# Kernel tuning notes

Hardware: AMD Instinct MI355X
Metric: run time of the kernel (lower is better)

## Reference

```python
import jax, jax.numpy as jnp
import numpy as np

B, N, D = 8, 1024, 512
H, DH = 8, 64
CH, CD = 6, 64  # ck/cv come in as (b, 6, n, 64); 6*64 = opn_inner_dim = 384
ID = H * DH    # inner_dim = 512
SCALE = DH ** -0.5


def _l2norm_dim1(x):
    # F.normalize(x, dim=1): normalize over the token axis of (b, n, c)
    return x / jnp.maximum(jnp.linalg.norm(x, axis=1, keepdims=True), 1e-12)


def _style_vectorizer(c, ws, bs):
    b, h, n, d = c.shape
    x = c.transpose(0, 2, 1, 3).reshape(b, n, h * d)
    x = _l2norm_dim1(x)
    for w, bi in zip(ws, bs):
        x = jax.nn.leaky_relu(x @ w.T + bi, 0.2)
    return x.reshape(b, n, H, DH).transpose(0, 2, 1, 3)


def _mlp_block(x, w, b):
    # x: (b, H, n, DH) -> rearr, normalize over n, Linear+GELU(exact), rearr back
    bb, h, n, d = x.shape
    y = x.transpose(0, 2, 1, 3).reshape(bb, n, h * d)
    y = _l2norm_dim1(y)
    y = jax.nn.gelu(y @ w.T + b, approximate=False)
    return y.reshape(bb, n, H, DH).transpose(0, 2, 1, 3)


def setup_inputs() -> dict:
    key = jax.random.key(0)
    ks = jax.random.split(key, 24)
    s = 0.02  # keep attention logits well-conditioned
    return {
        "x": jax.random.normal(ks[0], (B, N, D), jnp.float32),
        "ck": jax.random.normal(ks[1], (B, CH, N, CD), jnp.float32),
        "cv": jax.random.normal(ks[2], (B, CH, N, CD), jnp.float32),
        "w_qkv": jax.random.normal(ks[3], (3 * ID, D), jnp.float32) * s,
        "w_out": jax.random.normal(ks[4], (D, ID), jnp.float32) * s,
        "b_out": jnp.zeros((D,), jnp.float32),
        "ckw0": jax.random.normal(ks[5], (ID, CH * CD), jnp.float32) * s,
        "ckb0": jnp.zeros((ID,), jnp.float32),
        "ckw1": jax.random.normal(ks[6], (ID, ID), jnp.float32) * s,
        "ckb1": jnp.zeros((ID,), jnp.float32),
        "ckw2": jax.random.normal(ks[7], (ID, ID), jnp.float32) * s,
        "ckb2": jnp.zeros((ID,), jnp.float32),
        "cvw0": jax.random.normal(ks[8], (ID, CH * CD), jnp.float32) * s,
        "cvb0": jnp.zeros((ID,), jnp.float32),
        "cvw1": jax.random.normal(ks[9], (ID, ID), jnp.float32) * s,
        "cvb1": jnp.zeros((ID,), jnp.float32),
        "cvw2": jax.random.normal(ks[10], (ID, ID), jnp.float32) * s,
        "cvb2": jnp.zeros((ID,), jnp.float32),
        "nl_w": jax.random.normal(ks[11], (ID, ID), jnp.float32) * s,
        "nl_b": jnp.zeros((ID,), jnp.float32),
        "sub_ratio": jax.random.normal(ks[12], (1, H, 1, DH), jnp.float32) + 1.0,
    }


def reference(x, ck, cv, w_qkv, w_out, b_out,
              ckw0, ckb0, ckw1, ckb1, ckw2, ckb2,
              cvw0, cvb0, cvw1, cvb1, cvw2, cvb2,
              nl_w, nl_b, sub_ratio):
    b, n, _ = x.shape
    qkv = x @ w_qkv.T                      # (b, n, 3*ID)
    q, k, v = jnp.split(qkv, 3, axis=-1)
    to_h = lambda t: t.reshape(b, n, H, DH).transpose(0, 2, 1, 3)  # (b,H,n,DH)
    q, k, v = to_h(q), to_h(k), to_h(v)

    # standard self-attention branch
    dots = jnp.einsum("bhnd,bhmd->bhnm", q, k) * SCALE
    out = jnp.einsum("bhnm,bhmd->bhnd", jax.nn.softmax(dots, axis=-1), v)

    # context (correction) branch
    ckh = _style_vectorizer(ck, (ckw0, ckw1, ckw2), (ckb0, ckb1, ckb2))
    cvh = _style_vectorizer(cv, (cvw0, cvw1, cvw2), (cvb0, cvb1, cvb2))
    dots_c = jnp.einsum("bhnd,bhmd->bhnm", q, ckh) * SCALE
    out_c = jnp.einsum("bhnm,bhmd->bhnd", jax.nn.softmax(dots_c, axis=-1), cvh)
    out_c = _mlp_block(out_c, nl_w, nl_b)

    out = out - out_c * sub_ratio          # elementwise scale-subtract combine
    out = out.transpose(0, 2, 1, 3).reshape(b, n, ID)
    return out @ w_out.T + b_out
```

## Files before the change

### kernel.cpp

```cpp
#include <hip/hip_runtime.h>
#include <hip/hip_fp16.h>
#include <math.h>

typedef _Float16 h16_t;
typedef __attribute__((ext_vector_type(4))) _Float16 h16x4;
typedef __attribute__((ext_vector_type(8))) _Float16 h16x8;
typedef __attribute__((ext_vector_type(4))) float f32x4;

static_assert(sizeof(h16_t) == 2, "f16 size");

__device__ __forceinline__ f32x4 mfma16(h16x8 a, h16x8 b, f32x4 c) {
  return __builtin_amdgcn_mfma_f32_16x16x32_f16(a, b, c, 0, 0, 0);
}

struct CvtArgs {
  const float* src[10];
  h16_t* dst[10];
  int start4[10];
  int total4;
  int nblk_cvt;
  const float* c0;
  const float* c1;
  float* part;
};

__global__ __launch_bounds__(384) void k_cvt_p1(CvtArgs a) {
  const int bid = blockIdx.x;
  if (bid < a.nblk_cvt) {
    const int i4 = bid * 384 + threadIdx.x;
    if (i4 >= a.total4) return;
    int seg = 0;
#pragma unroll
    for (int t = 1; t < 10; ++t) seg += (i4 >= a.start4[t]) ? 1 : 0;
    const int off = (i4 - a.start4[seg]) * 4;
    const float4 v = *(const float4*)(a.src[seg] + off);
    h16x4 o;
    o[0] = (h16_t)v.x; o[1] = (h16_t)v.y; o[2] = (h16_t)v.z; o[3] = (h16_t)v.w;
    *(h16x4*)(a.dst[seg] + off) = o;
  } else {
    const int rid = bid - a.nblk_cvt;
    const int b = rid & 7, ch = (rid >> 3) & 63, z = rid >> 9;
    const int f = threadIdx.x;
    const float* c = z ? a.c1 : a.c0;
    const int h = f >> 6, d = f & 63;
    const float* p = c + ((size_t)(b * 6 + h) * 1024 + ch * 16) * 64 + d;
    float s = 0.f;
#pragma unroll
    for (int n = 0; n < 16; ++n) {
      const float v = p[(size_t)n * 64];
      s += v * v;
    }
    a.part[(size_t)z * 196608 + (size_t)(b * 64 + ch) * 384 + f] = s;
  }
}

template <int K>
__device__ __forceinline__ void gemm_run(const h16_t* __restrict__ A,
                                         const h16_t* __restrict__ W,
                                         int m0, int o0, h16_t* wl, f32x4* acc) {
  constexpr int NS = K / 128;
  const int lane = threadIdx.x & 63;
  const int l15 = lane & 15;
  const int quad = lane >> 4;
  int sr[4], sc[4], sd[4];
#pragma unroll
  for (int i = 0; i < 4; ++i) {
    const int id = threadIdx.x + i * 256;
    const int row = id >> 4, c = id & 15;
    sr[i] = row;
    sc[i] = c * 8;
    sd[i] = (row * 16 + (c ^ (row & 7))) * 8;
  }
  h16x8 wr[4];
#pragma unroll
  for (int i = 0; i < 4; ++i)
    wr[i] = *(const h16x8*)(W + (size_t)(o0 + sr[i]) * K + sc[i]);
#pragma unroll
  for (int i = 0; i < 4; ++i) *(h16x8*)(wl + sd[i]) = wr[i];
  __syncthreads();
#pragma unroll
  for (int sg = 0; sg < NS; ++sg) {
    if (sg + 1 < NS) {
#pragma unroll
      for (int i = 0; i < 4; ++i)
        wr[i] = *(const h16x8*)(W + (size_t)(o0 + sr[i]) * K + (sg + 1) * 128 + sc[i]);
    }
    const h16_t* ap = A + (size_t)(m0 + l15) * K + sg * 128 + quad * 8;
    const h16_t* wp = wl + (sg & 1) * 8192;
#pragma unroll
    for (int ks = 0; ks < 4; ++ks) {
      h16x8 af = *(const h16x8*)(ap + ks * 32);
#pragma unroll
      for (int j = 0; j < 4; ++j) {
        h16x8 wf = *(const h16x8*)(
            wp + (size_t)((j * 16 + l15) * 16 + ((ks * 4 + quad) ^ (l15 & 7))) * 8);
        acc[j] = mfma16(af, wf, acc[j]);
      }
    }
    if (sg + 1 < NS) {
      h16_t* wn = wl + ((sg + 1) & 1) * 8192;
#pragma unroll
      for (int i = 0; i < 4; ++i) *(h16x8*)(wn + sd[i]) = wr[i];
    }
    __syncthreads();
  }
}

#define EPILOGUE_SETUP()                            \
  const int wv = threadIdx.x >> 6;                  \
  const int lane = threadIdx.x & 63;                \
  const int l15 = lane & 15;                        \
  const int quad = lane >> 4;                       \
  const int m0 = blockIdx.x * 64 + wv * 16;         \
  const int o0 = blockIdx.y * 64;                   \
  f32x4 acc[4];                                     \
  for (int j = 0; j < 4; ++j) acc[j] = f32x4{0.f, 0.f, 0.f, 0.f};

struct Leaky2Args {
  const h16_t* A0; const h16_t* W0; const float* b0; h16_t* Y0;
  const h16_t* A1; const h16_t* W1; const float* b1; h16_t* Y1;
};

template <int K, int L0, int L1>
__global__ __launch_bounds__(256) void k_gemm_leaky2(Leaky2Args g) {
  __shared__ h16_t wl[2 * 8192];
  const int zz = blockIdx.z;
  const h16_t* A = zz ? g.A1 : g.A0;
  const h16_t* W = zz ? g.W1 : g.W0;
  const float* bias = zz ? g.b1 : g.b0;
  h16_t* Y = zz ? g.Y1 : g.Y0;
  EPILOGUE_SETUP();
  gemm_run<K>(A, W, m0, o0, wl, acc);
  const int LAYOUT = zz ? L1 : L0;
#pragma unroll
  for (int j = 0; j < 4; ++j)
#pragma unroll
    for (int r = 0; r < 4; ++r) {
      const int o = o0 + j * 16 + l15;
      const int m = m0 + quad * 4 + r;
      float v = acc[j][r] + bias[o];
      v = v > 0.f ? v : 0.2f * v;
      if (LAYOUT == 0) {
        Y[(size_t)m * 512 + o] = (h16_t)v;
      } else {
        const int b = m >> 10, n = m & 1023;
        const int h = o >> 6, d = o & 63;
        if (LAYOUT == 1)
          Y[((size_t)(b * 8 + h) * 1024 + n) * 64 + d] = (h16_t)v;
        else
          Y[((size_t)(b * 8 + h) * 64 + d) * 1024 + n] = (h16_t)v;
      }
    }
}

__global__ __launch_bounds__(256) void k_g0_qkv(
    Leaky2Args g, const h16_t* __restrict__ X, const h16_t* __restrict__ Wq,
    h16_t* __restrict__ qb, h16_t* __restrict__ kb, h16_t* __restrict__ vT) {
  __shared__ h16_t wl[2 * 8192];
  const int bid = blockIdx.x;
  const int wv = threadIdx.x >> 6;
  const int lane = threadIdx.x & 63;
  const int l15 = lane & 15;
  const int quad = lane >> 4;
  f32x4 acc[4];
#pragma unroll
  for (int j = 0; j < 4; ++j) acc[j] = f32x4{0.f, 0.f, 0.f, 0.f};

  if (bid < 2048) {
    const int zz = bid >> 10;
    const int m0 = (bid & 127) * 64 + wv * 16;
    const int o0 = ((bid >> 7) & 7) * 64;
    const h16_t* A = zz ? g.A1 : g.A0;
    const h16_t* W = zz ? g.W1 : g.W0;
    const float* bias = zz ? g.b1 : g.b0;
    h16_t* Y = zz ? g.Y1 : g.Y0;
    gemm_run<384>(A, W, m0, o0, wl, acc);
#pragma unroll
    for (int j = 0; j < 4; ++j)
#pragma unroll
      for (int r = 0; r < 4; ++r) {
        const int o = o0 + j * 16 + l15;
        const int m = m0 + quad * 4 + r;
        float v = acc[j][r] + bias[o];
        v = v > 0.f ? v : 0.2f * v;
        Y[(size_t)m * 512 + o] = (h16_t)v;
      }
  } else {
    const int q = bid - 2048;
    const int m0 = (q & 127) * 64 + wv * 16;
    const int o0 = (q >> 7) * 64;
    gemm_run<512>(X, Wq, m0, o0, wl, acc);
#pragma unroll
    for (int j = 0; j < 4; ++j)
#pragma unroll
      for (int r = 0; r < 4; ++r) {
        const int o = o0 + j * 16 + l15;
        const int m = m0 + quad * 4 + r;
        const int b = m >> 10, n = m & 1023;
        const int oo = o & 511, h = oo >> 6, d = oo & 63;
        const size_t bh = (size_t)(b * 8 + h);
        const h16_t v = (h16_t)acc[j][r];
        if (o < 512)
          qb[(bh * 1024 + n) * 64 + d] = v;
        else if (o < 1024)
          kb[(bh * 1024 + n) * 64 + d] = v;
        else
          vT[(bh * 64 + d) * 1024 + n] = v;
      }
  }
}

__global__ __launch_bounds__(256) void k_gemm_nl(
    const h16_t* __restrict__ A, const h16_t* __restrict__ W,
    const float* __restrict__ bias, const h16_t* __restrict__ attn,
    const float* __restrict__ subr, h16_t* __restrict__ Y) {
  __shared__ h16_t wl[2 * 8192];
  EPILOGUE_SETUP();
  gemm_run<512>(A, W, m0, o0, wl, acc);
#pragma unroll
  for (int j = 0; j < 4; ++j)
#pragma unroll
    for (int r = 0; r < 4; ++r) {
      const int o = o0 + j * 16 + l15;
      const int m = m0 + quad * 4 + r;
      const float v = acc[j][r] + bias[o];
      const float g = 0.5f * v * (1.f + erff(v * 0.70710678118654752f));
      const float res = (float)attn[(size_t)m * 512 + o] - g * subr[o];
      Y[(size_t)m * 512 + o] = (h16_t)res;
    }
}

__global__ __launch_bounds__(256) void k_gemm_out(
    const h16_t* __restrict__ A, const h16_t* __restrict__ W,
    const float* __restrict__ bias, float* __restrict__ Y) {
  __shared__ h16_t wl[2 * 8192];
  EPILOGUE_SETUP();
  gemm_run<512>(A, W, m0, o0, wl, acc);
#pragma unroll
  for (int j = 0; j < 4; ++j)
#pragma unroll
    for (int r = 0; r < 4; ++r) {
      const int o = o0 + j * 16 + l15;
      const int m = m0 + quad * 4 + r;
      Y[(size_t)m * 512 + o] = acc[j][r] + bias[o];
    }
}

__global__ __launch_bounds__(256) void k_attn4(
    const h16_t* __restrict__ q,
    const h16_t* __restrict__ k0, const h16_t* __restrict__ v0, h16_t* __restrict__ out0,
    const h16_t* __restrict__ k1, const h16_t* __restrict__ v1, h16_t* __restrict__ out1) {
  const int wv = threadIdx.x >> 6;
  const int lane = threadIdx.x & 63;
  const int l15 = lane & 15;
  const int quad = lane >> 4;
  const int bh = blockIdx.x, b = bh >> 3, h = bh & 7;
  const h16_t* kb = (blockIdx.z ? k1 : k0) + (size_t)bh * 65536;
  const h16_t* vb = (blockIdx.z ? v1 : v0) + (size_t)bh * 65536;
  h16_t* out = blockIdx.z ? out1 : out0;

  __shared__ h16_t kls[2 * 4096];
  __shared__ h16_t vls[2 * 4096];

  const int q0r = blockIdx.y * 128 + wv * 32;
  h16x8 qa[2][2];
#pragma unroll
  for (int t = 0; t < 2; ++t)
#pragma unroll
    for (int s = 0; s < 2; ++s)
      qa[t][s] = *(const h16x8*)(q + ((size_t)bh * 1024 + q0r + t * 16 + l15) * 64 + s * 32 + quad * 8);

  h16x8 ones;
#pragma unroll
  for (int j = 0; j < 8; ++j) ones[j] = (h16_t)1.f;

  int ksrc[2], vsrc[2], ldst[2];
#pragma unroll
  for (int i = 0; i < 2; ++i) {
    const int L = threadIdx.x + i * 256;
    const int row = L >> 3, cs = L & 7;
    const int key = ((row & 3) << 1) | ((row >> 3) & 1);
    const int c = cs ^ key;
    ksrc[i] = row * 64 + c * 8;
    vsrc[i] = row * 1024 + c * 8;
    ldst[i] = L * 8;
  }

  int kfo[2][4], vfo[2][4];
#pragma unroll
  for (int s = 0; s < 2; ++s)
#pragma unroll
    for (int nt = 0; nt < 4; ++nt) {
      const int r = (nt & 1) * 32 + (l15 >> 2) * 8 + (nt >> 1) * 4 + (l15 & 3);
      const int kk = ((r & 3) << 1) | ((r >> 3) & 1);
      kfo[s][nt] = (r * 8 + ((s * 4 + quad) ^ kk)) * 8;
      const int d = nt * 16 + l15;
      const int kd = ((d & 3) << 1) | ((d >> 3) & 1);
      vfo[s][nt] = (d * 8 + ((s * 4 + quad) ^ kd)) * 8;
    }

  f32x4 oaT[2][4];
#pragma unroll
  for (int t = 0; t < 2; ++t)
#pragma unroll
    for (int j = 0; j < 4; ++j) oaT[t][j] = f32x4{0.f, 0.f, 0.f, 0.f};
  f32x4 lacc[2];
#pragma unroll
  for (int t = 0; t < 2; ++t) lacc[t] = f32x4{0.f, 0.f, 0.f, 0.f};

  h16x8 kr[2], vr[2];
#pragma unroll
  for (int i = 0; i < 2; ++i) {
    kr[i] = *(const h16x8*)(kb + ksrc[i]);
    vr[i] = *(const h16x8*)(vb + vsrc[i]);
  }
#pragma unroll
  for (int i = 0; i < 2; ++i) {
    *(h16x8*)(kls + ldst[i]) = kr[i];
    *(h16x8*)(vls + ldst[i]) = vr[i];
  }
  __syncthreads();

  for (int mt = 0; mt < 16; ++mt) {
    const int cur = (mt & 1) * 4096;
    if (mt < 15) {
      const int mm1 = (mt + 1) * 64;
#pragma unroll
      for (int i = 0; i < 2; ++i) {
        kr[i] = *(const h16x8*)(kb + mm1 * 64 + ksrc[i]);
        vr[i] = *(const h16x8*)(vb + mm1 + vsrc[i]);
      }
    }

    f32x4 sfT[2][4];
#pragma unroll
    for (int t = 0; t < 2; ++t)
#pragma unroll
      for (int j = 0; j < 4; ++j) sfT[t][j] = f32x4{0.f, 0.f, 0.f, 0.f};
#pragma unroll
    for (int s = 0; s < 2; ++s)
#pragma unroll
      for (int nt = 0; nt < 4; ++nt) {
        h16x8 kf = *(const h16x8*)(kls + cur + kfo[s][nt]);
        sfT[0][nt] = mfma16(kf, qa[0][s], sfT[0][nt]);
        sfT[1][nt] = mfma16(kf, qa[1][s], sfT[1][nt]);
      }
    int pk[2][4][2];
#pragma unroll
    for (int t = 0; t < 2; ++t)
#pragma unroll
      for (int nt = 0; nt < 4; ++nt) {
        const float e0 = __expf(sfT[t][nt][0] * 0.125f);
        const float e1 = __expf(sfT[t][nt][1] * 0.125f);
        const float e2 = __expf(sfT[t][nt][2] * 0.125f);
        const float e3 = __expf(sfT[t][nt][3] * 0.125f);
        pk[t][nt][0] = __builtin_bit_cast(int, __builtin_amdgcn_cvt_pkrtz(e0, e1));
        pk[t][nt][1] = __builtin_bit_cast(int, __builtin_amdgcn_cvt_pkrtz(e2, e3));
      }
#pragma unroll
    for (int s = 0; s < 2; ++s) {
      int4 b0 = {pk[0][s][0], pk[0][s][1], pk[0][s + 2][0], pk[0][s + 2][1]};
      int4 b1 = {pk[1][s][0], pk[1][s][1], pk[1][s + 2][0], pk[1][s + 2][1]};
      h16x8 bf0 = __builtin_bit_cast(h16x8, b0);
      h16x8 bf1 = __builtin_bit_cast(h16x8, b1);
      lacc[0] = mfma16(ones, bf0, lacc[0]);
      lacc[1] = mfma16(ones, bf1, lacc[1]);
#pragma unroll
      for (int nt = 0; nt < 4; ++nt) {
        h16x8 vf = *(const h16x8*)(vls + cur + vfo[s][nt]);
        oaT[0][nt] = mfma16(vf, bf0, oaT[0][nt]);
        oaT[1][nt] = mfma16(vf, bf1, oaT[1][nt]);
      }
    }

    if (mt < 15) {
      const int nxt = ((mt + 1) & 1) * 4096;
#pragma unroll
      for (int i = 0; i < 2; ++i) {
        *(h16x8*)(kls + nxt + ldst[i]) = kr[i];
        *(h16x8*)(vls + nxt + ldst[i]) = vr[i];
      }
    }
    __syncthreads();
  }
#pragma unroll
  for (int t = 0; t < 2; ++t) {
    const float iv = 1.f / lacc[t][0];
    h16_t* obase = out + ((size_t)b * 1024 + q0r + t * 16 + l15) * 512 + h * 64 + quad * 4;
#pragma unroll
    for (int nt = 0; nt < 4; ++nt) {
      h16x4 o;
#pragma unroll
      for (int r = 0; r < 4; ++r) o[r] = (h16_t)(oaT[t][nt][r] * iv);
      *(h16x4*)(obase + nt * 16) = o;
    }
  }
}

__global__ __launch_bounds__(384) void k_cn_ck_p2(const float* __restrict__ part,
                                                  float* __restrict__ inv) {
  const int b = blockIdx.x, z = blockIdx.y, f = threadIdx.x;
  float s = 0.f;
#pragma unroll 8
  for (int ch = 0; ch < 64; ++ch)
    s += part[(size_t)z * 196608 + (size_t)(b * 64 + ch) * 384 + f];
  inv[z * 3072 + b * 384 + f] = 1.f / fmaxf(sqrtf(s), 1e-12f);
}

__global__ __launch_bounds__(384) void k_norm_ck(const float* __restrict__ c0,
                                                 const float* __restrict__ c1,
                                                 const float* __restrict__ inv,
                                                 h16_t* __restrict__ y0,
                                                 h16_t* __restrict__ y1) {
  const int bn = blockIdx.x, z = blockIdx.y, f = threadIdx.x;
  const float* c = z ? c1 : c0;
  h16_t* out = z ? y1 : y0;
  const int b = bn >> 10, n = bn & 1023;
  const int h = f >> 6, d = f & 63;
  out[(size_t)bn * 384 + f] =
      (h16_t)(c[((size_t)(b * 6 + h) * 1024 + n) * 64 + d] * inv[z * 3072 + b * 384 + f]);
}

__global__ __launch_bounds__(512) void k_cn_rm_p1(const h16_t* __restrict__ a,
                                                  float* __restrict__ part) {
  const int b = blockIdx.x, ch = blockIdx.y, f = threadIdx.x;
  const h16_t* p = a + ((size_t)b * 1024 + ch * 16) * 512 + f;
  float s = 0.f;
#pragma unroll
  for (int n = 0; n < 16; ++n) {
    const float v = (float)p[(size_t)n * 512];
    s += v * v;
  }
  part[(size_t)(b * 64 + ch) * 512 + f] = s;
}

__global__ __launch_bounds__(512) void k_cn_rm_p2(const float* __restrict__ part,
                                                  float* __restrict__ inv) {
  const int b = blockIdx.x, f = threadIdx.x;
  float s = 0.f;
#pragma unroll 8
  for (int ch = 0; ch < 64; ++ch) s += part[(size_t)(b * 64 + ch) * 512 + f];
  inv[b * 512 + f] = 1.f / fmaxf(sqrtf(s), 1e-12f);
}

__global__ __launch_bounds__(512) void k_norm_rm(const h16_t* __restrict__ a,
                                                 const float* __restrict__ inv,
                                                 h16_t* __restrict__ out) {
  const int bn = blockIdx.x, f = threadIdx.x;
  const int b = bn >> 10;
  out[(size_t)bn * 512 + f] = (h16_t)((float)a[(size_t)bn * 512 + f] * inv[b * 512 + f]);
}

extern "C" void kernel_launch(void* const* d_in, const int* in_sizes, int n_in,
                              void* d_out, int out_size, void* d_ws, size_t ws_size,
                              hipStream_t stream) {
  (void)in_sizes; (void)n_in; (void)out_size; (void)ws_size;
  const float* x     = (const float*)d_in[0];
  const float* ck    = (const float*)d_in[1];
  const float* cv    = (const float*)d_in[2];
  const float* w_qkv = (const float*)d_in[3];
  const float* w_out = (const float*)d_in[4];
  const float* b_out = (const float*)d_in[5];
  const float* ckw0  = (const float*)d_in[6];
  const float* ckb0  = (const float*)d_in[7];
  const float* ckw1  = (const float*)d_in[8];
  const float* ckb1  = (const float*)d_in[9];
  const float* ckw2  = (const float*)d_in[10];
  const float* ckb2  = (const float*)d_in[11];
  const float* cvw0  = (const float*)d_in[12];
  const float* cvb0  = (const float*)d_in[13];
  const float* cvw1  = (const float*)d_in[14];
  const float* cvb1  = (const float*)d_in[15];
  const float* cvw2  = (const float*)d_in[16];
  const float* cvb2  = (const float*)d_in[17];
  const float* nl_w  = (const float*)d_in[18];
  const float* nl_b  = (const float*)d_in[19];
  const float* subr  = (const float*)d_in[20];

  const size_t MB = 1024 * 1024;
  char* p = (char*)d_ws;
  float* inv1 = (float*)p;
  float* part = (float*)(p + 64 * 1024);
  h16_t* S0 = (h16_t*)(p + 2 * MB + 0 * 8 * MB);
  h16_t* S1 = (h16_t*)(p + 2 * MB + 1 * 8 * MB);
  h16_t* S2 = (h16_t*)(p + 2 * MB + 2 * 8 * MB);
  h16_t* S3 = (h16_t*)(p + 2 * MB + 3 * 8 * MB);
  h16_t* S4 = (h16_t*)(p + 2 * MB + 4 * 8 * MB);
  h16_t* S5 = (h16_t*)(p + 2 * MB + 5 * 8 * MB);
  h16_t* WBASE = (h16_t*)(p + 50 * MB);
  h16_t* w_qkvb = WBASE;
  h16_t* w_outb = w_qkvb + 786432;
  h16_t* ckw0b  = w_outb + 262144;
  h16_t* ckw1b  = ckw0b + 196608;
  h16_t* ckw2b  = ckw1b + 262144;
  h16_t* cvw0b  = ckw2b + 262144;
  h16_t* cvw1b  = cvw0b + 196608;
  h16_t* cvw2b  = cvw1b + 262144;
  h16_t* nl_wb  = cvw2b + 262144;
  h16_t* T0   = (h16_t*)d_out;
  h16_t* T1   = (h16_t*)d_out + 4194304;
  h16_t* XB   = S5;
  h16_t* ATTN = T0;

  const dim3 blk(256);
  {
    CvtArgs a;
    const float* srcs[10] = {x, w_qkv, w_out, ckw0, ckw1, ckw2, cvw0, cvw1, cvw2, nl_w};
    h16_t* dsts[10] = {XB, w_qkvb, w_outb, ckw0b, ckw1b, ckw2b, cvw0b, cvw1b, cvw2b, nl_wb};
    const int ns[10] = {4194304, 786432, 262144, 196608, 262144, 262144, 196608, 262144, 262144, 262144};
    int cum = 0;
    for (int i = 0; i < 10; ++i) {
      a.src[i] = srcs[i]; a.dst[i] = dsts[i]; a.start4[i] = cum; cum += ns[i] / 4;
    }
    a.total4 = cum;
    a.nblk_cvt = (cum + 383) / 384;
    a.c0 = ck; a.c1 = cv; a.part = part;
    k_cvt_p1<<<a.nblk_cvt + 1024, 384, 0, stream>>>(a);
  }

  k_cn_ck_p2<<<dim3(8, 2), 384, 0, stream>>>(part, inv1);
  k_norm_ck<<<dim3(8192, 2), 384, 0, stream>>>(ck, cv, inv1, T0, S0);

  {
    Leaky2Args g = {T0, ckw0b, ckb0, T1, S0, cvw0b, cvb0, S1};
    k_g0_qkv<<<5120, blk, 0, stream>>>(g, XB, w_qkvb, S2, S3, S4);
  }

  {
    Leaky2Args g = {T1, ckw1b, ckb1, T0, S1, cvw1b, cvb1, S0};
    k_gemm_leaky2<512, 0, 0><<<dim3(128, 8, 2), blk, 0, stream>>>(g);
  }
  {
    Leaky2Args g = {T0, ckw2b, ckb2, T1, S0, cvw2b, cvb2, S1};
    k_gemm_leaky2<512, 1, 2><<<dim3(128, 8, 2), blk, 0, stream>>>(g);
  }

  k_attn4<<<dim3(64, 8, 2), blk, 0, stream>>>(S2, S3, S4, ATTN, T1, S1, S5);

  k_cn_rm_p1<<<dim3(8, 64), 512, 0, stream>>>(S5, part);
  k_cn_rm_p2<<<8, 512, 0, stream>>>(part, inv1);
  k_norm_rm<<<8192, 512, 0, stream>>>(S5, inv1, S0);
  k_gemm_nl<<<dim3(128, 8), blk, 0, stream>>>(S0, nl_wb, nl_b, ATTN, subr, S1);
  k_gemm_out<<<dim3(128, 8), blk, 0, stream>>>(S1, w_outb, b_out, (float*)d_out);
}
```

Baseline: 344.9 us.

## Co-schedule self-attention with layer-1 GEMM and fuse column-norm reduction into ctx attention

The self-attention branch now runs in the same launch as the first hidden-layer GEMM of the context vectorizers, with block-id dispatch, so the two independent workloads can fill the GPU together. The context attention is split into its own kernel. Its epilogue accumulates per-column sums of squares through wave shuffles and atomics, which removes the separate pass that re-read the output to compute L2 norms. The cost is float atomic contention, non-deterministic summation order, and extra buffer reshuffling (ATTN now lives in S5, the ctx output in S3).

```diff
diff --git a/kernel.cpp b/kernel.cpp
--- a/kernel.cpp
+++ b/kernel.cpp
@@ -246,29 +246,24 @@
     }
 }
 
-__global__ __launch_bounds__(256) void k_attn4(
-    const h16_t* __restrict__ q,
-    const h16_t* __restrict__ k0, const h16_t* __restrict__ v0, h16_t* __restrict__ out0,
-    const h16_t* __restrict__ k1, const h16_t* __restrict__ v1, h16_t* __restrict__ out1) {
+template <bool SQ>
+__device__ void attn_body(h16_t* kls, h16_t* vls, const h16_t* __restrict__ qg,
+                          const h16_t* __restrict__ kb, const h16_t* __restrict__ vb,
+                          h16_t* __restrict__ out, int bh, int q0r0,
+                          float* part2) {
   const int wv = threadIdx.x >> 6;
   const int lane = threadIdx.x & 63;
   const int l15 = lane & 15;
   const int quad = lane >> 4;
-  const int bh = blockIdx.x, b = bh >> 3, h = bh & 7;
-  const h16_t* kb = (blockIdx.z ? k1 : k0) + (size_t)bh * 65536;
-  const h16_t* vb = (blockIdx.z ? v1 : v0) + (size_t)bh * 65536;
-  h16_t* out = blockIdx.z ? out1 : out0;
-
-  __shared__ h16_t kls[2 * 4096];
-  __shared__ h16_t vls[2 * 4096];
-
-  const int q0r = blockIdx.y * 128 + wv * 32;
+  const int b = bh >> 3, h = bh & 7;
+  const int q0r = q0r0 + wv * 32;
+
   h16x8 qa[2][2];
 #pragma unroll
   for (int t = 0; t < 2; ++t)
 #pragma unroll
     for (int s = 0; s < 2; ++s)
-      qa[t][s] = *(const h16x8*)(q + ((size_t)bh * 1024 + q0r + t * 16 + l15) * 64 + s * 32 + quad * 8);
+      qa[t][s] = *(const h16x8*)(qg + ((size_t)bh * 1024 + q0r + t * 16 + l15) * 64 + s * 32 + quad * 8);
 
   h16x8 ones;
 #pragma unroll
@@ -383,6 +378,14 @@
     }
     __syncthreads();
   }
+
+  float sq[4][4];
+  if (SQ) {
+#pragma unroll
+    for (int nt = 0; nt < 4; ++nt)
+#pragma unroll
+      for (int r = 0; r < 4; ++r) sq[nt][r] = 0.f;
+  }
 #pragma unroll
   for (int t = 0; t < 2; ++t) {
     const float iv = 1.f / lacc[t][0];
@@ -391,15 +394,86 @@
     for (int nt = 0; nt < 4; ++nt) {
       h16x4 o;
 #pragma unroll
-      for (int r = 0; r < 4; ++r) o[r] = (h16_t)(oaT[t][nt][r] * iv);
+      for (int r = 0; r < 4; ++r) {
+        const float v = oaT[t][nt][r] * iv;
+        o[r] = (h16_t)v;
+        if (SQ) sq[nt][r] += v * v;
+      }
       *(h16x4*)(obase + nt * 16) = o;
     }
   }
+  if (SQ) {
+#pragma unroll
+    for (int nt = 0; nt < 4; ++nt)
+#pragma unroll
+      for (int r = 0; r < 4; ++r) {
+        float s = sq[nt][r];
+        s += __shfl_xor(s, 1);
+        s += __shfl_xor(s, 2);
+        s += __shfl_xor(s, 4);
+        s += __shfl_xor(s, 8);
+        if (l15 == 0)
+          atomicAdd(&part2[b * 512 + h * 64 + nt * 16 + quad * 4 + r], s);
+      }
+  }
+}
+
+__global__ __launch_bounds__(256) void k_g1_attn(
+    Leaky2Args g, const h16_t* __restrict__ q, const h16_t* __restrict__ kb,
+    const h16_t* __restrict__ vT, h16_t* __restrict__ attn_out) {
+  __shared__ h16_t sm[16384];
+  const int bid = blockIdx.x;
+  if (bid < 2048) {
+    const int zz = bid >> 10;
+    const int rem = bid & 1023;
+    const int wv = threadIdx.x >> 6;
+    const int lane = threadIdx.x & 63;
+    const int l15 = lane & 15;
+    const int quad = lane >> 4;
+    const int m0 = (rem & 127) * 64 + wv * 16;
+    const int o0 = ((rem >> 7) & 7) * 64;
+    const h16_t* A = zz ? g.A1 : g.A0;
+    const h16_t* W = zz ? g.W1 : g.W0;
+    const float* bias = zz ? g.b1 : g.b0;
+    h16_t* Y = zz ? g.Y1 : g.Y0;
+    f32x4 acc[4];
+#pragma unroll
+    for (int j = 0; j < 4; ++j) acc[j] = f32x4{0.f, 0.f, 0.f, 0.f};
+    gemm_run<512>(A, W, m0, o0, sm, acc);
+#pragma unroll
+    for (int j = 0; j < 4; ++j)
+#pragma unroll
+      for (int r = 0; r < 4; ++r) {
+        const int o = o0 + j * 16 + l15;
+        const int m = m0 + quad * 4 + r;
+        float v = acc[j][r] + bias[o];
+        v = v > 0.f ? v : 0.2f * v;
+        Y[(size_t)m * 512 + o] = (h16_t)v;
+      }
+  } else {
+    const int aid = bid - 2048;
+    const int bh = aid & 63, qb = aid >> 6;
+    attn_body<false>(sm, sm + 8192, q, kb + (size_t)bh * 65536,
+                     vT + (size_t)bh * 65536, attn_out, bh, qb * 128, nullptr);
+  }
+}
+
+__global__ __launch_bounds__(256) void k_attn_ctx(
+    const h16_t* __restrict__ q, const h16_t* __restrict__ kc,
+    const h16_t* __restrict__ vc, h16_t* __restrict__ outc, float* part2) {
+  __shared__ h16_t sm[16384];
+  const int bh = blockIdx.x, qb = blockIdx.y;
+  attn_body<true>(sm, sm + 8192, q, kc + (size_t)bh * 65536,
+                  vc + (size_t)bh * 65536, outc, bh, qb * 128, part2);
 }
 
 __global__ __launch_bounds__(384) void k_cn_ck_p2(const float* __restrict__ part,
-                                                  float* __restrict__ inv) {
+                                                  float* __restrict__ inv,
+                                                  float* __restrict__ part2) {
   const int b = blockIdx.x, z = blockIdx.y, f = threadIdx.x;
+  if (z == 0) {
+    for (int t = f; t < 512; t += 384) part2[b * 512 + t] = 0.f;
+  }
   float s = 0.f;
 #pragma unroll 8
   for (int ch = 0; ch < 64; ++ch)
@@ -421,26 +495,10 @@
       (h16_t)(c[((size_t)(b * 6 + h) * 1024 + n) * 64 + d] * inv[z * 3072 + b * 384 + f]);
 }
 
-__global__ __launch_bounds__(512) void k_cn_rm_p1(const h16_t* __restrict__ a,
-                                                  float* __restrict__ part) {
-  const int b = blockIdx.x, ch = blockIdx.y, f = threadIdx.x;
-  const h16_t* p = a + ((size_t)b * 1024 + ch * 16) * 512 + f;
-  float s = 0.f;
-#pragma unroll
-  for (int n = 0; n < 16; ++n) {
-    const float v = (float)p[(size_t)n * 512];
-    s += v * v;
-  }
-  part[(size_t)(b * 64 + ch) * 512 + f] = s;
-}
-
-__global__ __launch_bounds__(512) void k_cn_rm_p2(const float* __restrict__ part,
-                                                  float* __restrict__ inv) {
+__global__ __launch_bounds__(512) void k_rm_p2b(const float* __restrict__ part2,
+                                                float* __restrict__ inv) {
   const int b = blockIdx.x, f = threadIdx.x;
-  float s = 0.f;
-#pragma unroll 8
-  for (int ch = 0; ch < 64; ++ch) s += part[(size_t)(b * 64 + ch) * 512 + f];
-  inv[b * 512 + f] = 1.f / fmaxf(sqrtf(s), 1e-12f);
+  inv[b * 512 + f] = 1.f / fmaxf(sqrtf(part2[b * 512 + f]), 1e-12f);
 }
 
 __global__ __launch_bounds__(512) void k_norm_rm(const h16_t* __restrict__ a,
@@ -481,6 +539,7 @@
   char* p = (char*)d_ws;
   float* inv1 = (float*)p;
   float* part = (float*)(p + 64 * 1024);
+  float* part2 = (float*)(p + 1600 * 1024);
   h16_t* S0 = (h16_t*)(p + 2 * MB + 0 * 8 * MB);
   h16_t* S1 = (h16_t*)(p + 2 * MB + 1 * 8 * MB);
   h16_t* S2 = (h16_t*)(p + 2 * MB + 2 * 8 * MB);
@@ -500,7 +559,7 @@
   h16_t* T0   = (h16_t*)d_out;
   h16_t* T1   = (h16_t*)d_out + 4194304;
   h16_t* XB   = S5;
-  h16_t* ATTN = T0;
+  h16_t* ATTN = S5;
 
   const dim3 blk(256);
   {
@@ -518,7 +577,7 @@
     k_cvt_p1<<<a.nblk_cvt + 1024, 384, 0, stream>>>(a);
   }
 
-  k_cn_ck_p2<<<dim3(8, 2), 384, 0, stream>>>(part, inv1);
+  k_cn_ck_p2<<<dim3(8, 2), 384, 0, stream>>>(part, inv1, part2);
   k_norm_ck<<<dim3(8192, 2), 384, 0, stream>>>(ck, cv, inv1, T0, S0);
 
   {
@@ -528,18 +587,18 @@
 
   {
     Leaky2Args g = {T1, ckw1b, ckb1, T0, S1, cvw1b, cvb1, S0};
-    k_gemm_leaky2<512, 0, 0><<<dim3(128, 8, 2), blk, 0, stream>>>(g);
-  }
+    k_g1_attn<<<2560, blk, 0, stream>>>(g, S2, S3, S4, ATTN);
+  }
+
   {
     Leaky2Args g = {T0, ckw2b, ckb2, T1, S0, cvw2b, cvb2, S1};
     k_gemm_leaky2<512, 1, 2><<<dim3(128, 8, 2), blk, 0, stream>>>(g);
   }
 
-  k_attn4<<<dim3(64, 8, 2), blk, 0, stream>>>(S2, S3, S4, ATTN, T1, S1, S5);
-
-  k_cn_rm_p1<<<dim3(8, 64), 512, 0, stream>>>(S5, part);
-  k_cn_rm_p2<<<8, 512, 0, stream>>>(part, inv1);
-  k_norm_rm<<<8192, 512, 0, stream>>>(S5, inv1, S0);
+  k_attn_ctx<<<dim3(64, 8), blk, 0, stream>>>(S2, T1, S1, S3, part2);
+
+  k_rm_p2b<<<8, 512, 0, stream>>>(part2, inv1);
+  k_norm_rm<<<8192, 512, 0, stream>>>(S3, inv1, S0);
   k_gemm_nl<<<dim3(128, 8), blk, 0, stream>>>(S0, nl_wb, nl_b, ATTN, subr, S1);
   k_gemm_out<<<dim3(128, 8), blk, 0, stream>>>(S1, w_outb, b_out, (float*)d_out);
 }
```

Result: no change. 346.5 us (+0.5%).

## Fuse column sum-of-squares into attention epilogue and read V directly from global

Applied to the files above, without the earlier changes.

The context-attention kernel now accumulates per-column squared norms of its output with wave shuffles and atomics into a buffer zeroed earlier. This removes the separate two-pass reduction kernel that re-read the attention output. The attention kernel also drops V staging in shared memory and loads V fragments straight from global memory inside the MFMA loop. That frees LDS and removes a copy, but it puts global-load latency in the inner loop and adds atomic contention.

```diff
diff --git a/kernel.cpp b/kernel.cpp
--- a/kernel.cpp
+++ b/kernel.cpp
@@ -249,7 +249,8 @@
 __global__ __launch_bounds__(256) void k_attn4(
     const h16_t* __restrict__ q,
     const h16_t* __restrict__ k0, const h16_t* __restrict__ v0, h16_t* __restrict__ out0,
-    const h16_t* __restrict__ k1, const h16_t* __restrict__ v1, h16_t* __restrict__ out1) {
+    const h16_t* __restrict__ k1, const h16_t* __restrict__ v1, h16_t* __restrict__ out1,
+    float* __restrict__ part2) {
   const int wv = threadIdx.x >> 6;
   const int lane = threadIdx.x & 63;
   const int l15 = lane & 15;
@@ -260,7 +261,6 @@
   h16_t* out = blockIdx.z ? out1 : out0;
 
   __shared__ h16_t kls[2 * 4096];
-  __shared__ h16_t vls[2 * 4096];
 
   const int q0r = blockIdx.y * 128 + wv * 32;
   h16x8 qa[2][2];
@@ -274,7 +274,7 @@
 #pragma unroll
   for (int j = 0; j < 8; ++j) ones[j] = (h16_t)1.f;
 
-  int ksrc[2], vsrc[2], ldst[2];
+  int ksrc[2], ldst[2];
 #pragma unroll
   for (int i = 0; i < 2; ++i) {
     const int L = threadIdx.x + i * 256;
@@ -282,11 +282,10 @@
     const int key = ((row & 3) << 1) | ((row >> 3) & 1);
     const int c = cs ^ key;
     ksrc[i] = row * 64 + c * 8;
-    vsrc[i] = row * 1024 + c * 8;
     ldst[i] = L * 8;
   }
 
-  int kfo[2][4], vfo[2][4];
+  int kfo[2][4];
 #pragma unroll
   for (int s = 0; s < 2; ++s)
 #pragma unroll
@@ -294,10 +293,9 @@
       const int r = (nt & 1) * 32 + (l15 >> 2) * 8 + (nt >> 1) * 4 + (l15 & 3);
       const int kk = ((r & 3) << 1) | ((r >> 3) & 1);
       kfo[s][nt] = (r * 8 + ((s * 4 + quad) ^ kk)) * 8;
-      const int d = nt * 16 + l15;
-      const int kd = ((d & 3) << 1) | ((d >> 3) & 1);
-      vfo[s][nt] = (d * 8 + ((s * 4 + quad) ^ kd)) * 8;
-    }
+    }
+
+  const h16_t* vrow = vb + (size_t)l15 * 1024 + quad * 8;
 
   f32x4 oaT[2][4];
 #pragma unroll
@@ -308,17 +306,11 @@
 #pragma unroll
   for (int t = 0; t < 2; ++t) lacc[t] = f32x4{0.f, 0.f, 0.f, 0.f};
 
-  h16x8 kr[2], vr[2];
-#pragma unroll
-  for (int i = 0; i < 2; ++i) {
-    kr[i] = *(const h16x8*)(kb + ksrc[i]);
-    vr[i] = *(const h16x8*)(vb + vsrc[i]);
-  }
-#pragma unroll
-  for (int i = 0; i < 2; ++i) {
-    *(h16x8*)(kls + ldst[i]) = kr[i];
-    *(h16x8*)(vls + ldst[i]) = vr[i];
-  }
+  h16x8 kr[2];
+#pragma unroll
+  for (int i = 0; i < 2; ++i) kr[i] = *(const h16x8*)(kb + ksrc[i]);
+#pragma unroll
+  for (int i = 0; i < 2; ++i) *(h16x8*)(kls + ldst[i]) = kr[i];
   __syncthreads();
 
   for (int mt = 0; mt < 16; ++mt) {
@@ -326,10 +318,7 @@
     if (mt < 15) {
       const int mm1 = (mt + 1) * 64;
 #pragma unroll
-      for (int i = 0; i < 2; ++i) {
-        kr[i] = *(const h16x8*)(kb + mm1 * 64 + ksrc[i]);
-        vr[i] = *(const h16x8*)(vb + mm1 + vsrc[i]);
-      }
+      for (int i = 0; i < 2; ++i) kr[i] = *(const h16x8*)(kb + mm1 * 64 + ksrc[i]);
     }
 
     f32x4 sfT[2][4];
@@ -367,7 +356,7 @@
       lacc[1] = mfma16(ones, bf1, lacc[1]);
 #pragma unroll
       for (int nt = 0; nt < 4; ++nt) {
-        h16x8 vf = *(const h16x8*)(vls + cur + vfo[s][nt]);
+        h16x8 vf = *(const h16x8*)(vrow + (size_t)nt * 16384 + mt * 64 + s * 32);
         oaT[0][nt] = mfma16(vf, bf0, oaT[0][nt]);
         oaT[1][nt] = mfma16(vf, bf1, oaT[1][nt]);
       }
@@ -376,12 +365,18 @@
     if (mt < 15) {
       const int nxt = ((mt + 1) & 1) * 4096;
 #pragma unroll
-      for (int i = 0; i < 2; ++i) {
-        *(h16x8*)(kls + nxt + ldst[i]) = kr[i];
-        *(h16x8*)(vls + nxt + ldst[i]) = vr[i];
-      }
+      for (int i = 0; i < 2; ++i) *(h16x8*)(kls + nxt + ldst[i]) = kr[i];
     }
     __syncthreads();
+  }
+
+  const bool SQ = blockIdx.z != 0;
+  float sq[4][4];
+  if (SQ) {
+#pragma unroll
+    for (int nt = 0; nt < 4; ++nt)
+#pragma unroll
+      for (int r = 0; r < 4; ++r) sq[nt][r] = 0.f;
   }
 #pragma unroll
   for (int t = 0; t < 2; ++t) {
@@ -391,15 +386,37 @@
     for (int nt = 0; nt < 4; ++nt) {
       h16x4 o;
 #pragma unroll
-      for (int r = 0; r < 4; ++r) o[r] = (h16_t)(oaT[t][nt][r] * iv);
+      for (int r = 0; r < 4; ++r) {
+        const float v = oaT[t][nt][r] * iv;
+        o[r] = (h16_t)v;
+        if (SQ) sq[nt][r] += v * v;
+      }
       *(h16x4*)(obase + nt * 16) = o;
     }
   }
+  if (SQ) {
+#pragma unroll
+    for (int nt = 0; nt < 4; ++nt)
+#pragma unroll
+      for (int r = 0; r < 4; ++r) {
+        float s = sq[nt][r];
+        s += __shfl_xor(s, 1);
+        s += __shfl_xor(s, 2);
+        s += __shfl_xor(s, 4);
+        s += __shfl_xor(s, 8);
+        if (l15 == 0)
+          atomicAdd(&part2[b * 512 + h * 64 + nt * 16 + quad * 4 + r], s);
+      }
+  }
 }
 
 __global__ __launch_bounds__(384) void k_cn_ck_p2(const float* __restrict__ part,
-                                                  float* __restrict__ inv) {
+                                                  float* __restrict__ inv,
+                                                  float* __restrict__ part2) {
   const int b = blockIdx.x, z = blockIdx.y, f = threadIdx.x;
+  if (z == 0) {
+    for (int t = f; t < 512; t += 384) part2[b * 512 + t] = 0.f;
+  }
   float s = 0.f;
 #pragma unroll 8
   for (int ch = 0; ch < 64; ++ch)
@@ -421,26 +438,10 @@
       (h16_t)(c[((size_t)(b * 6 + h) * 1024 + n) * 64 + d] * inv[z * 3072 + b * 384 + f]);
 }
 
-__global__ __launch_bounds__(512) void k_cn_rm_p1(const h16_t* __restrict__ a,
-                                                  float* __restrict__ part) {
-  const int b = blockIdx.x, ch = blockIdx.y, f = threadIdx.x;
-  const h16_t* p = a + ((size_t)b * 1024 + ch * 16) * 512 + f;
-  float s = 0.f;
-#pragma unroll
-  for (int n = 0; n < 16; ++n) {
-    const float v = (float)p[(size_t)n * 512];
-    s += v * v;
-  }
-  part[(size_t)(b * 64 + ch) * 512 + f] = s;
-}
-
-__global__ __launch_bounds__(512) void k_cn_rm_p2(const float* __restrict__ part,
-                                                  float* __restrict__ inv) {
+__global__ __launch_bounds__(512) void k_rm_p2b(const float* __restrict__ part2,
+                                                float* __restrict__ inv) {
   const int b = blockIdx.x, f = threadIdx.x;
-  float s = 0.f;
-#pragma unroll 8
-  for (int ch = 0; ch < 64; ++ch) s += part[(size_t)(b * 64 + ch) * 512 + f];
-  inv[b * 512 + f] = 1.f / fmaxf(sqrtf(s), 1e-12f);
+  inv[b * 512 + f] = 1.f / fmaxf(sqrtf(part2[b * 512 + f]), 1e-12f);
 }
 
 __global__ __launch_bounds__(512) void k_norm_rm(const h16_t* __restrict__ a,
@@ -481,6 +482,7 @@
   char* p = (char*)d_ws;
   float* inv1 = (float*)p;
   float* part = (float*)(p + 64 * 1024);
+  float* part2 = (float*)(p + 1600 * 1024);
   h16_t* S0 = (h16_t*)(p + 2 * MB + 0 * 8 * MB);
   h16_t* S1 = (h16_t*)(p + 2 * MB + 1 * 8 * MB);
   h16_t* S2 = (h16_t*)(p + 2 * MB + 2 * 8 * MB);
@@ -518,7 +520,7 @@
     k_cvt_p1<<<a.nblk_cvt + 1024, 384, 0, stream>>>(a);
   }
 
-  k_cn_ck_p2<<<dim3(8, 2), 384, 0, stream>>>(part, inv1);
+  k_cn_ck_p2<<<dim3(8, 2), 384, 0, stream>>>(part, inv1, part2);
   k_norm_ck<<<dim3(8192, 2), 384, 0, stream>>>(ck, cv, inv1, T0, S0);
 
   {
@@ -530,15 +532,15 @@
     Leaky2Args g = {T1, ckw1b, ckb1, T0, S1, cvw1b, cvb1, S0};
     k_gemm_leaky2<512, 0, 0><<<dim3(128, 8, 2), blk, 0, stream>>>(g);
   }
+
   {
     Leaky2Args g = {T0, ckw2b, ckb2, T1, S0, cvw2b, cvb2, S1};
     k_gemm_leaky2<512, 1, 2><<<dim3(128, 8, 2), blk, 0, stream>>>(g);
   }
 
-  k_attn4<<<dim3(64, 8, 2), blk, 0, stream>>>(S2, S3, S4, ATTN, T1, S1, S5);
-
-  k_cn_rm_p1<<<dim3(8, 64), 512, 0, stream>>>(S5, part);
-  k_cn_rm_p2<<<8, 512, 0, stream>>>(part, inv1);
+  k_attn4<<<dim3(64, 8, 2), blk, 0, stream>>>(S2, S3, S4, ATTN, T1, S1, S5, part2);
+
+  k_rm_p2b<<<8, 512, 0, stream>>>(part2, inv1);
   k_norm_rm<<<8192, 512, 0, stream>>>(S5, inv1, S0);
   k_gemm_nl<<<dim3(128, 8), blk, 0, stream>>>(S0, nl_wb, nl_b, ATTN, subr, S1);
   k_gemm_out<<<dim3(128, 8), blk, 0, stream>>>(S1, w_outb, b_out, (float*)d_out);
```

Result: slower. 391.3 us (+13.5%).
